# Performance work log

Measured on AMD Instinct MI355X. Metric: run time of the kernel, lower is better.

The kernel has to match this reference:

```python
import jax, jax.numpy as jnp
import numpy as np

NUM_HEADS = 12
D = 768
HD = D // NUM_HEADS  # 64

def setup_inputs() -> dict:
    key = jax.random.key(0)
    ks = jax.random.split(key, 9)
    s = 0.02
    return {
        "x": jax.random.normal(ks[0], (4, 2048, D), dtype=jnp.float32),
        "QW_w": jax.random.normal(ks[1], (D, D), dtype=jnp.float32) * s,
        "QW_b": jax.random.normal(ks[2], (D,), dtype=jnp.float32) * s,
        "KW_w": jax.random.normal(ks[3], (D, D), dtype=jnp.float32) * s,
        "KW_b": jax.random.normal(ks[4], (D,), dtype=jnp.float32) * s,
        "VW_w": jax.random.normal(ks[5], (D, D), dtype=jnp.float32) * s,
        "VW_b": jax.random.normal(ks[6], (D,), dtype=jnp.float32) * s,
        "OW_w": jax.random.normal(ks[7], (D, D), dtype=jnp.float32) * s,
        "OW_b": jax.random.normal(ks[8], (D,), dtype=jnp.float32) * s,
    }

def reference(x, QW_w, QW_b, KW_w, KW_b, VW_w, VW_b, OW_w, OW_b):
    b, s, _ = x.shape
    # torch nn.Linear: y = x @ W.T + b
    def proj(w, bias):
        y = jnp.einsum('bsd,ed->bse', x, w) + bias
        return y.reshape(b, s, NUM_HEADS, HD).transpose(0, 2, 1, 3)  # [b,h,s,hd]
    q = proj(QW_w, QW_b)
    k = proj(KW_w, KW_b)
    v = proj(VW_w, VW_b)
    scores = jnp.einsum('bhqd,bhkd->bhqk', q, k) / jnp.sqrt(jnp.float32(HD))
    attn = jax.nn.softmax(scores, axis=-1)
    out = jnp.einsum('bhqk,bhkd->bhqd', attn, v)
    out = out.transpose(0, 2, 1, 3).reshape(b, s, NUM_HEADS * HD)
    return jnp.einsum('bsd,ed->bse', out, OW_w) + OW_b
```

## Files before the change

### kernel.cpp

```cpp
#include <hip/hip_runtime.h>
#include <hip/hip_bf16.h>

#define NH  12
#define HD  64
#define DIM 768
#define SEQ 2048
#define NB  4
#define MM  (NB*SEQ)
#define NKB (SEQ/64)

typedef short    v8s  __attribute__((ext_vector_type(8)));
typedef float    v4f  __attribute__((ext_vector_type(4)));
typedef float    v16f __attribute__((ext_vector_type(16)));
typedef unsigned v4u  __attribute__((ext_vector_type(4)));

#if __has_builtin(__builtin_amdgcn_exp2f)
#define EXP2(x) __builtin_amdgcn_exp2f(x)
#else
#define EXP2(x) __builtin_exp2f(x)
#endif

static __device__ __forceinline__ unsigned short f2b(float f) {
    unsigned int u = __float_as_uint(f);
    return (unsigned short)((u + 0x7FFFu + ((u >> 16) & 1u)) >> 16);
}
static __device__ __forceinline__ unsigned pk2bf(float lo, float hi) {
    return __builtin_amdgcn_perm(__float_as_uint(hi) + 0x8000u,
                                 __float_as_uint(lo) + 0x8000u, 0x07060302u);
}
static __device__ __forceinline__ void g2l16(const unsigned short* g, unsigned short* l) {
    __builtin_amdgcn_global_load_lds(
        (const __attribute__((address_space(1))) void*)g,
        (__attribute__((address_space(3))) void*)l, 16, 0, 0);
}

__global__ void cast_f32_bf16(const float* __restrict__ in,
                              unsigned short* __restrict__ out, int n4) {
    int i = blockIdx.x * blockDim.x + threadIdx.x;
    if (i < n4) {
        float4 v = reinterpret_cast<const float4*>(in)[i];
        ushort4 o;
        o.x = f2b(v.x); o.y = f2b(v.y); o.z = f2b(v.z); o.w = f2b(v.w);
        reinterpret_cast<ushort4*>(out)[i] = o;
    }
}

__global__ void cast4_f32_bf16(const float* __restrict__ i0, const float* __restrict__ i1,
                               const float* __restrict__ i2, const float* __restrict__ i3,
                               unsigned short* __restrict__ o0, unsigned short* __restrict__ o1,
                               unsigned short* __restrict__ o2, unsigned short* __restrict__ o3,
                               int n4) {
    int i = blockIdx.x * blockDim.x + threadIdx.x;
    if (i >= n4) return;
    const float* in; unsigned short* out;
    switch (blockIdx.y) {
        case 0: in = i0; out = o0; break;
        case 1: in = i1; out = o1; break;
        case 2: in = i2; out = o2; break;
        default: in = i3; out = o3; break;
    }
    float4 v = reinterpret_cast<const float4*>(in)[i];
    ushort4 o;
    o.x = f2b(v.x); o.y = f2b(v.y); o.z = f2b(v.z); o.w = f2b(v.w);
    reinterpret_cast<ushort4*>(out)[i] = o;
}

static __device__ __forceinline__ void gemm_core_128(
    const unsigned short* __restrict__ A,
    const unsigned short* __restrict__ W,
    int m0, int n0l,
    unsigned short* As, unsigned short* Bs,
    v4f acc[4][4])
{
    const int tid  = threadIdx.x;
    const int w    = tid >> 6, lane = tid & 63;
    const int quad = lane >> 4, l16 = lane & 15;
    const int wm   = w & 1,  wn = w >> 1;
    const int lane8 = lane >> 3, sc = lane & 7;

    #pragma unroll
    for (int i = 0; i < 4; ++i)
        #pragma unroll
        for (int j = 0; j < 4; ++j)
            acc[i][j] = v4f{0.f, 0.f, 0.f, 0.f};

    for (int kb = 0; kb < DIM; kb += 64) {
        __syncthreads();
        #pragma unroll
        for (int t = 0; t < 4; ++t) {
            int r8 = w * 32 + t * 8;
            int r  = r8 + lane8;
            int gch = sc ^ (r & 7);
            g2l16(&A[(size_t)(m0  + r) * DIM + kb + gch * 8], &As[r8 * 64]);
            g2l16(&W[(size_t)(n0l + r) * DIM + kb + gch * 8], &Bs[r8 * 64]);
        }
        __syncthreads();
        #pragma unroll
        for (int kk = 0; kk < 64; kk += 32) {
            v8s a[4], b[4];
            int chb = kk >> 3;
            #pragma unroll
            for (int i = 0; i < 4; ++i) {
                int m = wm * 64 + i * 16 + l16;
                a[i] = *reinterpret_cast<const v8s*>(
                    &As[m * 64 + (((chb + quad) ^ (m & 7)) << 3)]);
                int n = wn * 64 + i * 16 + l16;
                b[i] = *reinterpret_cast<const v8s*>(
                    &Bs[n * 64 + (((chb + quad) ^ (n & 7)) << 3)]);
            }
            #pragma unroll
            for (int i = 0; i < 4; ++i)
                #pragma unroll
                for (int j = 0; j < 4; ++j)
                    acc[i][j] = __builtin_amdgcn_mfma_f32_16x16x32_bf16(a[i], b[j], acc[i][j], 0, 0, 0);
        }
    }
}

__global__ __launch_bounds__(256) void gemm_qkv(
    const unsigned short* __restrict__ A,
    const unsigned short* __restrict__ Wq,
    const unsigned short* __restrict__ Wk,
    const unsigned short* __restrict__ Wv,
    const float* __restrict__ bq,
    const float* __restrict__ bk,
    const float* __restrict__ bvp,
    unsigned short* __restrict__ Qb,
    unsigned short* __restrict__ Kb,
    unsigned short* __restrict__ Vf)
{
    __shared__ __align__(16) unsigned short As[128 * 64];
    __shared__ __align__(16) unsigned short Bs[128 * 64];

    const int m0   = blockIdx.x * 128;
    const int by   = blockIdx.y;
    const int wsel = by / 6;
    const int n0l  = (by % 6) * 128;
    const unsigned short* W    = (wsel == 0) ? Wq : (wsel == 1) ? Wk : Wv;
    const float*          bias = (wsel == 0) ? bq : (wsel == 1) ? bk : bvp;
    const float scale = (wsel == 0) ? 0.1803368801f : 1.0f;

    v4f acc[4][4];
    gemm_core_128(A, W, m0, n0l, As, Bs, acc);

    const int tid  = threadIdx.x;
    const int w    = tid >> 6, lane = tid & 63;
    const int quad = lane >> 4, l16 = lane & 15;
    const int wm   = w & 1,  wn = w >> 1;

    #pragma unroll
    for (int i = 0; i < 4; ++i) {
        #pragma unroll
        for (int j = 0; j < 4; ++j) {
            int gnl = n0l + wn * 64 + j * 16 + l16;
            float bias_v = bias[gnl];
            int h = gnl >> 6, hd = gnl & 63;
            if (wsel == 2) {
                int gm0 = m0 + wm * 64 + i * 16 + quad * 4;
                int bb = gm0 >> 11, s0k = gm0 & (SEQ - 1);
                int kbi = s0k >> 6;
                int halfv = quad >> 1, j0 = (quad & 1) * 4;
                int hb = hd >> 5, l31v = hd & 31;
                ushort4 pkv;
                pkv.x = f2b(acc[i][j][0] + bias_v);
                pkv.y = f2b(acc[i][j][1] + bias_v);
                pkv.z = f2b(acc[i][j][2] + bias_v);
                pkv.w = f2b(acc[i][j][3] + bias_v);
                size_t frag = ((size_t)(bb * NH + h) * NKB + kbi) * 8 + hb * 4 + i;
                *reinterpret_cast<ushort4*>(
                    &Vf[frag * 512 + (halfv * 32 + l31v) * 8 + j0]) = pkv;
            } else {
                unsigned short* out = (wsel == 0) ? Qb : Kb;
                #pragma unroll
                for (int r = 0; r < 4; ++r) {
                    int gm = m0 + wm * 64 + i * 16 + quad * 4 + r;
                    int bb = gm >> 11, s = gm & (SEQ - 1);
                    out[((size_t)(bb * NH + h) * SEQ + s) * HD + hd] =
                        f2b((acc[i][j][r] + bias_v) * scale);
                }
            }
        }
    }
}

__global__ __launch_bounds__(256) void gemm_o(
    const unsigned short* __restrict__ A,
    const unsigned short* __restrict__ W,
    const float* __restrict__ bias,
    float* __restrict__ out)
{
    __shared__ __align__(16) unsigned short As[128 * 64];
    __shared__ __align__(16) unsigned short Bs[128 * 64];

    const int m0  = blockIdx.x * 128;
    const int n0l = blockIdx.y * 128;

    v4f acc[4][4];
    gemm_core_128(A, W, m0, n0l, As, Bs, acc);

    const int tid  = threadIdx.x;
    const int w    = tid >> 6, lane = tid & 63;
    const int quad = lane >> 4, l16 = lane & 15;
    const int wm   = w & 1,  wn = w >> 1;

    #pragma unroll
    for (int i = 0; i < 4; ++i) {
        #pragma unroll
        for (int j = 0; j < 4; ++j) {
            int gn = n0l + wn * 64 + j * 16 + l16;
            float bias_v = bias[gn];
            #pragma unroll
            for (int r = 0; r < 4; ++r) {
                int gm = m0 + wm * 64 + i * 16 + quad * 4 + r;
                out[(size_t)gm * DIM + gn] = acc[i][j][r] + bias_v;
            }
        }
    }
}

__global__ __launch_bounds__(256, 3) void attn(
    const unsigned short* __restrict__ Q,
    const unsigned short* __restrict__ K,
    const unsigned short* __restrict__ Vf,
    unsigned short* __restrict__ ctx)
{
    __shared__ __align__(16) unsigned short Ks[2][64 * 64];

    const int tid  = threadIdx.x;
    const int w    = tid >> 6, lane = tid & 63;
    const int l31  = lane & 31, half = lane >> 5;
    const int lane8 = lane >> 3, sc = lane & 7;
    const int bh   = blockIdx.y;
    const int b    = bh / NH, h = bh % NH;
    const int q0   = blockIdx.x * 128 + w * 32;

    const unsigned short* Qp = Q  + ((size_t)bh * SEQ + q0) * HD;
    const unsigned short* Kp = K  + (size_t)bh * SEQ * HD;
    const unsigned short* Vh = Vf + (size_t)bh * NKB * 8 * 512 + lane * 8;

    v8s bq[4];
    #pragma unroll
    for (int c = 0; c < 4; ++c)
        bq[c] = *reinterpret_cast<const v8s*>(&Qp[l31 * HD + c * 16 + half * 8]);

    v8s va[2][4];
    #pragma unroll
    for (int hb = 0; hb < 2; ++hb)
        #pragma unroll
        for (int c = 0; c < 4; ++c)
            va[hb][c] = *reinterpret_cast<const v8s*>(&Vh[(hb * 4 + c) * 512]);

    v16f o0, o1, Z;
    #pragma unroll
    for (int i = 0; i < 16; ++i) { o0[i] = 0.f; o1[i] = 0.f; Z[i] = 0.f; }
    float li = 0.f;

    const int rx = l31 & 7;
    int rdoff[4];
    #pragma unroll
    for (int c = 0; c < 4; ++c)
        rdoff[c] = l31 * 64 + (((c * 2 + half) ^ rx) << 3);

    #define STAGE_K(kb_, buf_)                                                       \
        do {                                                                         \
            _Pragma("unroll")                                                        \
            for (int t = 0; t < 2; ++t) {                                            \
                int r8  = (t * 4 + w) * 8;                                           \
                int row = r8 + lane8;                                                \
                int gch = sc ^ (row & 7);                                            \
                g2l16(&Kp[(size_t)((kb_) + row) * HD + gch * 8], &Ks[buf_][r8 * 64]);\
            }                                                                        \
        } while (0)

    STAGE_K(0, 0);

    for (int it = 0; it < NKB; ++it) {
        const int buf = it & 1;
        __syncthreads();
        if (it + 1 < NKB) STAGE_K((it + 1) * 64, buf ^ 1);

        v16f s0, s1;
        {
            v8s ka00 = *reinterpret_cast<const v8s*>(&Ks[buf][rdoff[0]]);
            v8s ka10 = *reinterpret_cast<const v8s*>(&Ks[buf][rdoff[0] + 2048]);
            s0 = __builtin_amdgcn_mfma_f32_32x32x16_bf16(ka00, bq[0], Z, 0, 0, 0);
            s1 = __builtin_amdgcn_mfma_f32_32x32x16_bf16(ka10, bq[0], Z, 0, 0, 0);
            #pragma unroll
            for (int c = 1; c < 4; ++c) {
                v8s k0 = *reinterpret_cast<const v8s*>(&Ks[buf][rdoff[c]]);
                v8s k1 = *reinterpret_cast<const v8s*>(&Ks[buf][rdoff[c] + 2048]);
                s0 = __builtin_amdgcn_mfma_f32_32x32x16_bf16(k0, bq[c], s0, 0, 0, 0);
                s1 = __builtin_amdgcn_mfma_f32_32x32x16_bf16(k1, bq[c], s1, 0, 0, 0);
            }
        }

        unsigned pk[8][2];
        #pragma unroll
        for (int g = 0; g < 4; ++g) {
            float e0 = EXP2(s0[4*g+0]), e1 = EXP2(s0[4*g+1]);
            float e2 = EXP2(s0[4*g+2]), e3 = EXP2(s0[4*g+3]);
            li += (e0 + e1) + (e2 + e3);
            pk[g][0] = pk2bf(e0, e1);
            pk[g][1] = pk2bf(e2, e3);
            float f0 = EXP2(s1[4*g+0]), f1 = EXP2(s1[4*g+1]);
            float f2 = EXP2(s1[4*g+2]), f3 = EXP2(s1[4*g+3]);
            li += (f0 + f1) + (f2 + f3);
            pk[4+g][0] = pk2bf(f0, f1);
            pk[4+g][1] = pk2bf(f2, f3);
        }

        #pragma unroll
        for (int cp = 0; cp < 4; ++cp) {
            unsigned a0 = pk[2*cp][0],   a1 = pk[2*cp][1];
            unsigned b0 = pk[2*cp+1][0], b1 = pk[2*cp+1][1];
            unsigned u0 = half ? a0 : b0;
            unsigned u1 = half ? a1 : b1;
            unsigned x0 = __shfl_xor(u0, 32);
            unsigned x1 = __shfl_xor(u1, 32);
            v4u fw;
            fw.x = half ? x0 : a0;
            fw.y = half ? x1 : a1;
            fw.z = half ? b0 : x0;
            fw.w = half ? b1 : x1;
            v8s pf = __builtin_bit_cast(v8s, fw);
            o0 = __builtin_amdgcn_mfma_f32_32x32x16_bf16(va[0][cp], pf, o0, 0, 0, 0);
            o1 = __builtin_amdgcn_mfma_f32_32x32x16_bf16(va[1][cp], pf, o1, 0, 0, 0);
        }

        if (it + 1 < NKB) {
            const unsigned short* Vn = Vh + (size_t)(it + 1) * 8 * 512;
            #pragma unroll
            for (int hb = 0; hb < 2; ++hb)
                #pragma unroll
                for (int c = 0; c < 4; ++c)
                    va[hb][c] = *reinterpret_cast<const v8s*>(&Vn[(hb * 4 + c) * 512]);
        }
    }
    #undef STAGE_K

    float inv = 1.0f / (li + __shfl_xor(li, 32));

    const int q = q0 + l31;
    size_t base = ((size_t)(b * SEQ + q)) * DIM + h * HD;
    #pragma unroll
    for (int g = 0; g < 4; ++g) {
        int hd0 = 8 * g + 4 * half;
        uint2 u0, u1;
        u0.x = pk2bf(o0[4*g+0] * inv, o0[4*g+1] * inv);
        u0.y = pk2bf(o0[4*g+2] * inv, o0[4*g+3] * inv);
        u1.x = pk2bf(o1[4*g+0] * inv, o1[4*g+1] * inv);
        u1.y = pk2bf(o1[4*g+2] * inv, o1[4*g+3] * inv);
        *reinterpret_cast<uint2*>(&ctx[base + hd0])      = u0;
        *reinterpret_cast<uint2*>(&ctx[base + 32 + hd0]) = u1;
    }
}

extern "C" void kernel_launch(void* const* d_in, const int* in_sizes, int n_in,
                              void* d_out, int out_size, void* d_ws, size_t ws_size,
                              hipStream_t stream) {
    const float* x  = (const float*)d_in[0];
    const float* qw = (const float*)d_in[1]; const float* qb = (const float*)d_in[2];
    const float* kw = (const float*)d_in[3]; const float* kb = (const float*)d_in[4];
    const float* vw = (const float*)d_in[5]; const float* vb = (const float*)d_in[6];
    const float* ow = (const float*)d_in[7]; const float* ob = (const float*)d_in[8];
    float* out = (float*)d_out;

    char* ws = (char*)d_ws;
    size_t off = 0;
    auto alloc = [&](size_t bytes) -> unsigned short* {
        unsigned short* p = (unsigned short*)(ws + off);
        off += (bytes + 255) & ~(size_t)255;
        return p;
    };
    const size_t XB = (size_t)MM * DIM * 2;
    const size_t WB = (size_t)DIM * DIM * 2;
    const size_t QB = (size_t)NB * NH * SEQ * HD * 2;

    unsigned short* xb  = alloc(XB);
    unsigned short* wqb = alloc(WB);
    unsigned short* wkb = alloc(WB);
    unsigned short* wvb = alloc(WB);
    unsigned short* wob = alloc(WB);
    unsigned short* Qb  = alloc(QB);
    unsigned short* Kb  = alloc(QB);
    unsigned short* Vfb = alloc(QB);
    unsigned short* ctx = alloc(XB);

    const int n4x = MM * DIM / 4;
    const int n4w = DIM * DIM / 4;
    cast_f32_bf16<<<(n4x + 255) / 256, 256, 0, stream>>>(x, xb, n4x);
    cast4_f32_bf16<<<dim3((n4w + 255) / 256, 4), 256, 0, stream>>>(
        qw, kw, vw, ow, wqb, wkb, wvb, wob, n4w);

    gemm_qkv<<<dim3(MM / 128, 18), 256, 0, stream>>>(
        xb, wqb, wkb, wvb, qb, kb, vb, Qb, Kb, Vfb);

    attn<<<dim3(SEQ / 128, NB * NH), 256, 0, stream>>>(Qb, Kb, Vfb, ctx);

    gemm_o<<<dim3(MM / 128, DIM / 128), 256, 0, stream>>>(ctx, wob, ob, out);
}
```

Before: 234.1 us.

## Fuse Q/K/V projections per head and double-buffer V prefetch in attention

The QKV GEMM now computes all three projections for one head in a single block, so each 128-row A tile is loaded into LDS once instead of three times. The grid shrinks from 18 to 12 column blocks, and each block carries three 64-wide B tiles plus a larger accumulator set. The attention loop is unrolled by two with ping-pong V register buffers, so the next V fragments are issued before the current tile's MFMAs instead of after. The risks are more registers and LDS per block, lower occupancy, and fewer blocks in the GEMM grid.

```diff
diff --git a/kernel.cpp b/kernel.cpp
--- a/kernel.cpp
+++ b/kernel.cpp
@@ -65,59 +65,7 @@
     reinterpret_cast<ushort4*>(out)[i] = o;
 }
 
-static __device__ __forceinline__ void gemm_core_128(
-    const unsigned short* __restrict__ A,
-    const unsigned short* __restrict__ W,
-    int m0, int n0l,
-    unsigned short* As, unsigned short* Bs,
-    v4f acc[4][4])
-{
-    const int tid  = threadIdx.x;
-    const int w    = tid >> 6, lane = tid & 63;
-    const int quad = lane >> 4, l16 = lane & 15;
-    const int wm   = w & 1,  wn = w >> 1;
-    const int lane8 = lane >> 3, sc = lane & 7;
-
-    #pragma unroll
-    for (int i = 0; i < 4; ++i)
-        #pragma unroll
-        for (int j = 0; j < 4; ++j)
-            acc[i][j] = v4f{0.f, 0.f, 0.f, 0.f};
-
-    for (int kb = 0; kb < DIM; kb += 64) {
-        __syncthreads();
-        #pragma unroll
-        for (int t = 0; t < 4; ++t) {
-            int r8 = w * 32 + t * 8;
-            int r  = r8 + lane8;
-            int gch = sc ^ (r & 7);
-            g2l16(&A[(size_t)(m0  + r) * DIM + kb + gch * 8], &As[r8 * 64]);
-            g2l16(&W[(size_t)(n0l + r) * DIM + kb + gch * 8], &Bs[r8 * 64]);
-        }
-        __syncthreads();
-        #pragma unroll
-        for (int kk = 0; kk < 64; kk += 32) {
-            v8s a[4], b[4];
-            int chb = kk >> 3;
-            #pragma unroll
-            for (int i = 0; i < 4; ++i) {
-                int m = wm * 64 + i * 16 + l16;
-                a[i] = *reinterpret_cast<const v8s*>(
-                    &As[m * 64 + (((chb + quad) ^ (m & 7)) << 3)]);
-                int n = wn * 64 + i * 16 + l16;
-                b[i] = *reinterpret_cast<const v8s*>(
-                    &Bs[n * 64 + (((chb + quad) ^ (n & 7)) << 3)]);
-            }
-            #pragma unroll
-            for (int i = 0; i < 4; ++i)
-                #pragma unroll
-                for (int j = 0; j < 4; ++j)
-                    acc[i][j] = __builtin_amdgcn_mfma_f32_16x16x32_bf16(a[i], b[j], acc[i][j], 0, 0, 0);
-        }
-    }
-}
-
-__global__ __launch_bounds__(256) void gemm_qkv(
+__global__ __launch_bounds__(256, 3) void gemm_qkv(
     const unsigned short* __restrict__ A,
     const unsigned short* __restrict__ Wq,
     const unsigned short* __restrict__ Wk,
@@ -130,55 +78,114 @@
     unsigned short* __restrict__ Vf)
 {
     __shared__ __align__(16) unsigned short As[128 * 64];
-    __shared__ __align__(16) unsigned short Bs[128 * 64];
-
-    const int m0   = blockIdx.x * 128;
-    const int by   = blockIdx.y;
-    const int wsel = by / 6;
-    const int n0l  = (by % 6) * 128;
-    const unsigned short* W    = (wsel == 0) ? Wq : (wsel == 1) ? Wk : Wv;
-    const float*          bias = (wsel == 0) ? bq : (wsel == 1) ? bk : bvp;
-    const float scale = (wsel == 0) ? 0.1803368801f : 1.0f;
-
-    v4f acc[4][4];
-    gemm_core_128(A, W, m0, n0l, As, Bs, acc);
+    __shared__ __align__(16) unsigned short Bs[3][64 * 64];
 
     const int tid  = threadIdx.x;
     const int w    = tid >> 6, lane = tid & 63;
     const int quad = lane >> 4, l16 = lane & 15;
     const int wm   = w & 1,  wn = w >> 1;
-
-    #pragma unroll
-    for (int i = 0; i < 4; ++i) {
-        #pragma unroll
-        for (int j = 0; j < 4; ++j) {
-            int gnl = n0l + wn * 64 + j * 16 + l16;
-            float bias_v = bias[gnl];
-            int h = gnl >> 6, hd = gnl & 63;
-            if (wsel == 2) {
-                int gm0 = m0 + wm * 64 + i * 16 + quad * 4;
-                int bb = gm0 >> 11, s0k = gm0 & (SEQ - 1);
-                int kbi = s0k >> 6;
-                int halfv = quad >> 1, j0 = (quad & 1) * 4;
-                int hb = hd >> 5, l31v = hd & 31;
-                ushort4 pkv;
-                pkv.x = f2b(acc[i][j][0] + bias_v);
-                pkv.y = f2b(acc[i][j][1] + bias_v);
-                pkv.z = f2b(acc[i][j][2] + bias_v);
-                pkv.w = f2b(acc[i][j][3] + bias_v);
-                size_t frag = ((size_t)(bb * NH + h) * NKB + kbi) * 8 + hb * 4 + i;
-                *reinterpret_cast<ushort4*>(
-                    &Vf[frag * 512 + (halfv * 32 + l31v) * 8 + j0]) = pkv;
-            } else {
-                unsigned short* out = (wsel == 0) ? Qb : Kb;
+    const int lane8 = lane >> 3, sc = lane & 7;
+    const int m0   = blockIdx.x * 128;
+    const int h    = blockIdx.y;
+    const int n0   = h * 64;
+
+    v4f acc[3][4][2];
+    #pragma unroll
+    for (int s = 0; s < 3; ++s)
+        #pragma unroll
+        for (int i = 0; i < 4; ++i)
+            #pragma unroll
+            for (int j = 0; j < 2; ++j)
+                acc[s][i][j] = v4f{0.f, 0.f, 0.f, 0.f};
+
+    for (int kb = 0; kb < DIM; kb += 64) {
+        __syncthreads();
+        #pragma unroll
+        for (int t = 0; t < 4; ++t) {
+            int r8 = w * 32 + t * 8;
+            int r  = r8 + lane8;
+            int gch = sc ^ (r & 7);
+            g2l16(&A[(size_t)(m0 + r) * DIM + kb + gch * 8], &As[r8 * 64]);
+        }
+        #pragma unroll
+        for (int u = 0; u < 6; ++u) {
+            int G = w * 6 + u;
+            int set = G >> 3, rg = G & 7;
+            int row = rg * 8 + lane8;
+            int gch = sc ^ (row & 7);
+            const unsigned short* Wp = (set == 0) ? Wq : (set == 1) ? Wk : Wv;
+            g2l16(&Wp[(size_t)(n0 + row) * DIM + kb + gch * 8], &Bs[set][rg * 8 * 64]);
+        }
+        __syncthreads();
+        #pragma unroll
+        for (int kk = 0; kk < 64; kk += 32) {
+            int chb = kk >> 3;
+            v8s a[4];
+            #pragma unroll
+            for (int i = 0; i < 4; ++i) {
+                int m = wm * 64 + i * 16 + l16;
+                a[i] = *reinterpret_cast<const v8s*>(
+                    &As[m * 64 + (((chb + quad) ^ (m & 7)) << 3)]);
+            }
+            #pragma unroll
+            for (int s = 0; s < 3; ++s) {
+                v8s b[2];
+                #pragma unroll
+                for (int j = 0; j < 2; ++j) {
+                    int n = wn * 32 + j * 16 + l16;
+                    b[j] = *reinterpret_cast<const v8s*>(
+                        &Bs[s][n * 64 + (((chb + quad) ^ (n & 7)) << 3)]);
+                }
+                #pragma unroll
+                for (int i = 0; i < 4; ++i)
+                    #pragma unroll
+                    for (int j = 0; j < 2; ++j)
+                        acc[s][i][j] = __builtin_amdgcn_mfma_f32_16x16x32_bf16(
+                            a[i], b[j], acc[s][i][j], 0, 0, 0);
+            }
+        }
+    }
+
+    #pragma unroll
+    for (int s = 0; s < 2; ++s) {
+        unsigned short* out = s ? Kb : Qb;
+        const float* bias   = s ? bk : bq;
+        const float scale   = s ? 1.0f : 0.1803368801f;
+        #pragma unroll
+        for (int i = 0; i < 4; ++i) {
+            #pragma unroll
+            for (int j = 0; j < 2; ++j) {
+                int hd = wn * 32 + j * 16 + l16;
+                float bias_v = bias[n0 + hd];
                 #pragma unroll
                 for (int r = 0; r < 4; ++r) {
                     int gm = m0 + wm * 64 + i * 16 + quad * 4 + r;
-                    int bb = gm >> 11, s = gm & (SEQ - 1);
-                    out[((size_t)(bb * NH + h) * SEQ + s) * HD + hd] =
-                        f2b((acc[i][j][r] + bias_v) * scale);
+                    int bb = gm >> 11, sq = gm & (SEQ - 1);
+                    out[((size_t)(bb * NH + h) * SEQ + sq) * HD + hd] =
+                        f2b((acc[s][i][j][r] + bias_v) * scale);
                 }
             }
+        }
+    }
+    #pragma unroll
+    for (int i = 0; i < 4; ++i) {
+        #pragma unroll
+        for (int j = 0; j < 2; ++j) {
+            int hd = wn * 32 + j * 16 + l16;
+            int hb = hd >> 5, l31v = hd & 31;
+            float bias_v = bvp[n0 + hd];
+            int gm0 = m0 + wm * 64 + i * 16 + quad * 4;
+            int bb = gm0 >> 11, sk = gm0 & (SEQ - 1);
+            int kbi = sk >> 6;
+            int halfv = quad >> 1, j0 = (quad & 1) * 4;
+            ushort4 pkv;
+            pkv.x = f2b(acc[2][i][j][0] + bias_v);
+            pkv.y = f2b(acc[2][i][j][1] + bias_v);
+            pkv.z = f2b(acc[2][i][j][2] + bias_v);
+            pkv.w = f2b(acc[2][i][j][3] + bias_v);
+            size_t frag = ((size_t)(bb * NH + h) * NKB + kbi) * 8 + hb * 4 + i;
+            *reinterpret_cast<ushort4*>(
+                &Vf[frag * 512 + (halfv * 32 + l31v) * 8 + j0]) = pkv;
         }
     }
 }
@@ -192,16 +199,52 @@
     __shared__ __align__(16) unsigned short As[128 * 64];
     __shared__ __align__(16) unsigned short Bs[128 * 64];
 
-    const int m0  = blockIdx.x * 128;
-    const int n0l = blockIdx.y * 128;
-
-    v4f acc[4][4];
-    gemm_core_128(A, W, m0, n0l, As, Bs, acc);
-
     const int tid  = threadIdx.x;
     const int w    = tid >> 6, lane = tid & 63;
     const int quad = lane >> 4, l16 = lane & 15;
     const int wm   = w & 1,  wn = w >> 1;
+    const int lane8 = lane >> 3, sc = lane & 7;
+    const int m0  = blockIdx.x * 128;
+    const int n0l = blockIdx.y * 128;
+
+    v4f acc[4][4];
+    #pragma unroll
+    for (int i = 0; i < 4; ++i)
+        #pragma unroll
+        for (int j = 0; j < 4; ++j)
+            acc[i][j] = v4f{0.f, 0.f, 0.f, 0.f};
+
+    for (int kb = 0; kb < DIM; kb += 64) {
+        __syncthreads();
+        #pragma unroll
+        for (int t = 0; t < 4; ++t) {
+            int r8 = w * 32 + t * 8;
+            int r  = r8 + lane8;
+            int gch = sc ^ (r & 7);
+            g2l16(&A[(size_t)(m0  + r) * DIM + kb + gch * 8], &As[r8 * 64]);
+            g2l16(&W[(size_t)(n0l + r) * DIM + kb + gch * 8], &Bs[r8 * 64]);
+        }
+        __syncthreads();
+        #pragma unroll
+        for (int kk = 0; kk < 64; kk += 32) {
+            v8s a[4], b[4];
+            int chb = kk >> 3;
+            #pragma unroll
+            for (int i = 0; i < 4; ++i) {
+                int m = wm * 64 + i * 16 + l16;
+                a[i] = *reinterpret_cast<const v8s*>(
+                    &As[m * 64 + (((chb + quad) ^ (m & 7)) << 3)]);
+                int n = wn * 64 + i * 16 + l16;
+                b[i] = *reinterpret_cast<const v8s*>(
+                    &Bs[n * 64 + (((chb + quad) ^ (n & 7)) << 3)]);
+            }
+            #pragma unroll
+            for (int i = 0; i < 4; ++i)
+                #pragma unroll
+                for (int j = 0; j < 4; ++j)
+                    acc[i][j] = __builtin_amdgcn_mfma_f32_16x16x32_bf16(a[i], b[j], acc[i][j], 0, 0, 0);
+        }
+    }
 
     #pragma unroll
     for (int i = 0; i < 4; ++i) {
@@ -243,7 +286,7 @@
     for (int c = 0; c < 4; ++c)
         bq[c] = *reinterpret_cast<const v8s*>(&Qp[l31 * HD + c * 16 + half * 8]);
 
-    v8s va[2][4];
+    v8s va[2][4], vb[2][4];
     #pragma unroll
     for (int hb = 0; hb < 2; ++hb)
         #pragma unroll
@@ -272,70 +315,72 @@
             }                                                                        \
         } while (0)
 
+    #define TILE(IT, BUF, VCUR, VNEXT)                                               \
+    {                                                                                \
+        __syncthreads();                                                             \
+        if ((IT) + 1 < NKB) {                                                        \
+            STAGE_K(((IT) + 1) * 64, (BUF) ^ 1);                                     \
+            const unsigned short* Vn = Vh + (size_t)((IT) + 1) * 8 * 512;            \
+            _Pragma("unroll")                                                        \
+            for (int hb = 0; hb < 2; ++hb)                                           \
+                _Pragma("unroll")                                                    \
+                for (int c = 0; c < 4; ++c)                                          \
+                    VNEXT[hb][c] = *reinterpret_cast<const v8s*>(&Vn[(hb*4+c)*512]); \
+        }                                                                            \
+        v16f s0, s1;                                                                 \
+        {                                                                            \
+            v8s ka0 = *reinterpret_cast<const v8s*>(&Ks[BUF][rdoff[0]]);             \
+            v8s ka1 = *reinterpret_cast<const v8s*>(&Ks[BUF][rdoff[0] + 2048]);      \
+            s0 = __builtin_amdgcn_mfma_f32_32x32x16_bf16(ka0, bq[0], Z, 0, 0, 0);    \
+            s1 = __builtin_amdgcn_mfma_f32_32x32x16_bf16(ka1, bq[0], Z, 0, 0, 0);    \
+            _Pragma("unroll")                                                        \
+            for (int c = 1; c < 4; ++c) {                                            \
+                v8s k0 = *reinterpret_cast<const v8s*>(&Ks[BUF][rdoff[c]]);          \
+                v8s k1 = *reinterpret_cast<const v8s*>(&Ks[BUF][rdoff[c] + 2048]);   \
+                s0 = __builtin_amdgcn_mfma_f32_32x32x16_bf16(k0, bq[c], s0, 0, 0, 0);\
+                s1 = __builtin_amdgcn_mfma_f32_32x32x16_bf16(k1, bq[c], s1, 0, 0, 0);\
+            }                                                                        \
+        }                                                                            \
+        unsigned pk[8][2];                                                           \
+        _Pragma("unroll")                                                            \
+        for (int g = 0; g < 4; ++g) {                                                \
+            float e0 = EXP2(s0[4*g+0]), e1 = EXP2(s0[4*g+1]);                        \
+            float e2 = EXP2(s0[4*g+2]), e3 = EXP2(s0[4*g+3]);                        \
+            li += (e0 + e1) + (e2 + e3);                                             \
+            pk[g][0] = pk2bf(e0, e1);                                                \
+            pk[g][1] = pk2bf(e2, e3);                                                \
+            float f0 = EXP2(s1[4*g+0]), f1 = EXP2(s1[4*g+1]);                        \
+            float f2 = EXP2(s1[4*g+2]), f3 = EXP2(s1[4*g+3]);                        \
+            li += (f0 + f1) + (f2 + f3);                                             \
+            pk[4+g][0] = pk2bf(f0, f1);                                              \
+            pk[4+g][1] = pk2bf(f2, f3);                                              \
+        }                                                                            \
+        _Pragma("unroll")                                                            \
+        for (int cp = 0; cp < 4; ++cp) {                                             \
+            unsigned a0 = pk[2*cp][0],   a1 = pk[2*cp][1];                           \
+            unsigned b0 = pk[2*cp+1][0], b1 = pk[2*cp+1][1];                         \
+            unsigned u0 = half ? a0 : b0;                                            \
+            unsigned u1 = half ? a1 : b1;                                            \
+            unsigned x0 = __shfl_xor(u0, 32);                                        \
+            unsigned x1 = __shfl_xor(u1, 32);                                        \
+            v4u fw;                                                                  \
+            fw.x = half ? x0 : a0;                                                   \
+            fw.y = half ? x1 : a1;                                                   \
+            fw.z = half ? b0 : x0;                                                   \
+            fw.w = half ? b1 : x1;                                                   \
+            v8s pf = __builtin_bit_cast(v8s, fw);                                    \
+            o0 = __builtin_amdgcn_mfma_f32_32x32x16_bf16(VCUR[0][cp], pf, o0, 0,0,0);\
+            o1 = __builtin_amdgcn_mfma_f32_32x32x16_bf16(VCUR[1][cp], pf, o1, 0,0,0);\
+        }                                                                            \
+    }
+
     STAGE_K(0, 0);
 
-    for (int it = 0; it < NKB; ++it) {
-        const int buf = it & 1;
-        __syncthreads();
-        if (it + 1 < NKB) STAGE_K((it + 1) * 64, buf ^ 1);
-
-        v16f s0, s1;
-        {
-            v8s ka00 = *reinterpret_cast<const v8s*>(&Ks[buf][rdoff[0]]);
-            v8s ka10 = *reinterpret_cast<const v8s*>(&Ks[buf][rdoff[0] + 2048]);
-            s0 = __builtin_amdgcn_mfma_f32_32x32x16_bf16(ka00, bq[0], Z, 0, 0, 0);
-            s1 = __builtin_amdgcn_mfma_f32_32x32x16_bf16(ka10, bq[0], Z, 0, 0, 0);
-            #pragma unroll
-            for (int c = 1; c < 4; ++c) {
-                v8s k0 = *reinterpret_cast<const v8s*>(&Ks[buf][rdoff[c]]);
-                v8s k1 = *reinterpret_cast<const v8s*>(&Ks[buf][rdoff[c] + 2048]);
-                s0 = __builtin_amdgcn_mfma_f32_32x32x16_bf16(k0, bq[c], s0, 0, 0, 0);
-                s1 = __builtin_amdgcn_mfma_f32_32x32x16_bf16(k1, bq[c], s1, 0, 0, 0);
-            }
-        }
-
-        unsigned pk[8][2];
-        #pragma unroll
-        for (int g = 0; g < 4; ++g) {
-            float e0 = EXP2(s0[4*g+0]), e1 = EXP2(s0[4*g+1]);
-            float e2 = EXP2(s0[4*g+2]), e3 = EXP2(s0[4*g+3]);
-            li += (e0 + e1) + (e2 + e3);
-            pk[g][0] = pk2bf(e0, e1);
-            pk[g][1] = pk2bf(e2, e3);
-            float f0 = EXP2(s1[4*g+0]), f1 = EXP2(s1[4*g+1]);
-            float f2 = EXP2(s1[4*g+2]), f3 = EXP2(s1[4*g+3]);
-            li += (f0 + f1) + (f2 + f3);
-            pk[4+g][0] = pk2bf(f0, f1);
-            pk[4+g][1] = pk2bf(f2, f3);
-        }
-
-        #pragma unroll
-        for (int cp = 0; cp < 4; ++cp) {
-            unsigned a0 = pk[2*cp][0],   a1 = pk[2*cp][1];
-            unsigned b0 = pk[2*cp+1][0], b1 = pk[2*cp+1][1];
-            unsigned u0 = half ? a0 : b0;
-            unsigned u1 = half ? a1 : b1;
-            unsigned x0 = __shfl_xor(u0, 32);
-            unsigned x1 = __shfl_xor(u1, 32);
-            v4u fw;
-            fw.x = half ? x0 : a0;
-            fw.y = half ? x1 : a1;
-            fw.z = half ? b0 : x0;
-            fw.w = half ? b1 : x1;
-            v8s pf = __builtin_bit_cast(v8s, fw);
-            o0 = __builtin_amdgcn_mfma_f32_32x32x16_bf16(va[0][cp], pf, o0, 0, 0, 0);
-            o1 = __builtin_amdgcn_mfma_f32_32x32x16_bf16(va[1][cp], pf, o1, 0, 0, 0);
-        }
-
-        if (it + 1 < NKB) {
-            const unsigned short* Vn = Vh + (size_t)(it + 1) * 8 * 512;
-            #pragma unroll
-            for (int hb = 0; hb < 2; ++hb)
-                #pragma unroll
-                for (int c = 0; c < 4; ++c)
-                    va[hb][c] = *reinterpret_cast<const v8s*>(&Vn[(hb * 4 + c) * 512]);
-        }
-    }
+    for (int it = 0; it < NKB; it += 2) {
+        TILE(it,     0, va, vb)
+        TILE(it + 1, 1, vb, va)
+    }
+    #undef TILE
     #undef STAGE_K
 
     float inv = 1.0f / (li + __shfl_xor(li, 32));
@@ -392,7 +437,7 @@
     cast4_f32_bf16<<<dim3((n4w + 255) / 256, 4), 256, 0, stream>>>(
         qw, kw, vw, ow, wqb, wkb, wvb, wob, n4w);
 
-    gemm_qkv<<<dim3(MM / 128, 18), 256, 0, stream>>>(
+    gemm_qkv<<<dim3(MM / 128, NH), 256, 0, stream>>>(
         xb, wqb, wkb, wvb, qb, kb, vb, Qb, Kb, Vfb);
 
     attn<<<dim3(SEQ / 128, NB * NH), 256, 0, stream>>>(Qb, Kb, Vfb, ctx);
```

Measured after the change: 228.7 us. 2.3% less time.
